# Kernel tuning notes

Measured on AMD Instinct MI355X. Metric: run time of the kernel, lower is better.

The kernel has to match this reference:

```python
import jax, jax.numpy as jnp
import numpy as np

B, T, D, H = 4, 2048, 1024, 16
HD = D // H  # 64


def setup_inputs() -> dict:
    key = jax.random.key(0)
    ks = jax.random.split(key, 6)
    s = 0.02
    return {
        "embed": jax.random.normal(ks[0], (B, T, D), dtype=jnp.float32),
        "mask": jnp.ones((1, 1, 1, T), dtype=jnp.int32),
        "Wq": jax.random.normal(ks[1], (D, D), dtype=jnp.float32) * s,
        "bq": jnp.zeros((D,), dtype=jnp.float32),
        "Wk": jax.random.normal(ks[2], (D, D), dtype=jnp.float32) * s,
        "bk": jnp.zeros((D,), dtype=jnp.float32),
        "Wv": jax.random.normal(ks[3], (D, D), dtype=jnp.float32) * s,
        "bv": jnp.zeros((D,), dtype=jnp.float32),
        "Wo": jax.random.normal(ks[4], (D, D), dtype=jnp.float32) * s,
        "bo": jnp.zeros((D,), dtype=jnp.float32),
    }


def _attn(embed, Wq, bq, Wk, bk, Wv, bv, Wo, bo, mask):
    b, t, _ = embed.shape
    q = (embed @ Wq + bq).reshape(b, t, H, HD).transpose(0, 2, 1, 3)  # [B,H,T,hd]
    k = (embed @ Wk + bk).reshape(b, t, H, HD).transpose(0, 2, 1, 3)
    v = (embed @ Wv + bv).reshape(b, t, H, HD).transpose(0, 2, 1, 3)
    scores = jnp.einsum("bhqd,bhkd->bhqk", q, k) * (1.0 / np.sqrt(HD))
    scores = jnp.where(mask == 0, jnp.float32(-jnp.inf), scores)
    weights = jax.nn.softmax(scores, axis=-1)  # dropout p=0 in eval
    ctx = jnp.einsum("bhqk,bhkd->bhqd", weights, v)
    merged = ctx.transpose(0, 2, 1, 3).reshape(b, t, D)
    return merged @ Wo + bo


def reference(embed, mask, Wq, bq, Wk, bk, Wv, bv, Wo, bo):
    return _attn(embed, Wq, bq, Wk, bk, Wv, bv, Wo, bo, mask)
```

## Files before the change

### kernel.cpp

```cpp
#include <hip/hip_runtime.h>


typedef __bf16 bf16_t;
typedef bf16_t bf16x8 __attribute__((ext_vector_type(8)));
typedef float  f32x4  __attribute__((ext_vector_type(4)));
typedef unsigned u32x4 __attribute__((ext_vector_type(4)));
typedef unsigned short u16x8 __attribute__((ext_vector_type(8)));
typedef unsigned short u16x4 __attribute__((ext_vector_type(4)));

#define DEV static __device__ __forceinline__

constexpr int Bc = 4, Tc = 2048, Dc = 1024, Hc = 16, HDc = 64;
constexpr int Mc = Bc * Tc;
constexpr int NQKV = 3 * Dc;

DEV unsigned short f2bf(float f) {
  union { float f; unsigned u; } v; v.f = f;
  return (unsigned short)((v.u + 0x7fffu + ((v.u >> 16) & 1u)) >> 16);
}

DEV void gload_lds16(const void* g, const void* ldsbase) {
  unsigned m0v = __builtin_amdgcn_readfirstlane((unsigned)(unsigned long long)ldsbase);
  asm volatile("s_mov_b32 m0, %0\n\t"
               "global_load_lds_dwordx4 %1, off"
               :: "s"(m0v), "v"(g) : "memory");
}

DEV f32x4 mfma16(bf16x8 a, bf16x8 b, f32x4 c) {
  return __builtin_amdgcn_mfma_f32_16x16x32_bf16(a, b, c, 0, 0, 0);
}

DEV void pl32swap(unsigned& a, unsigned& b) {
  asm("v_permlane32_swap_b32 %0, %1" : "+v"(a), "+v"(b));
}
DEV void pl16swap(unsigned& a, unsigned& b) {
  asm("v_permlane16_swap_b32 %0, %1" : "+v"(a), "+v"(b));
}

DEV int fragaddr(int row, int col) {
  return (row >> 4) * 1024 + ((col >> 5) << 9) + (((col >> 3) & 3) << 7)
       + ((row & 15) << 3) + (col & 7);
}

__global__ __launch_bounds__(256) void prep(const float* __restrict__ embed,
                                            const float* __restrict__ Wq,
                                            const float* __restrict__ Wk,
                                            const float* __restrict__ Wv,
                                            const float* __restrict__ Wo,
                                            const float* __restrict__ bq,
                                            const float* __restrict__ bk,
                                            const float* __restrict__ bv,
                                            unsigned short* __restrict__ embed_bf,
                                            unsigned short* __restrict__ WtAll,
                                            float* __restrict__ ball) {
  __shared__ unsigned short tile[64 * 80];
  const int bb = blockIdx.x;
  const int tid = threadIdx.x;

  if (bb < 8192) {
    int i = bb * 256 + tid;
    float4 v = ((const float4*)embed)[i];
    u16x4 o = { f2bf(v.x), f2bf(v.y), f2bf(v.z), f2bf(v.w) };
    *(u16x4*)(embed_bf + (size_t)i * 4) = o;
    return;
  }
  if (bb < 8192 + 1024) {
    int wb = bb - 8192;
    int bx = wb & 15, by = (wb >> 4) & 15, bz = wb >> 8;
    const float* W = bz == 0 ? Wq : bz == 1 ? Wk : bz == 2 ? Wv : Wo;
    unsigned short* dst = WtAll + (size_t)bz * 1024 * 1024;
    const int kb = by * 64, nb = bx * 64;
#pragma unroll
    for (int i = 0; i < 4; i++) {
      int ci = i * 256 + tid;
      int r = ci >> 4, c4 = ci & 15;
      float4 v = *(const float4*)(W + (size_t)(kb + r) * 1024 + nb + c4 * 4);
      u16x4 o = { f2bf(v.x), f2bf(v.y), f2bf(v.z), f2bf(v.w) };
      *(u16x4*)(tile + r * 80 + c4 * 4) = o;
    }
    __syncthreads();
#pragma unroll
    for (int i = 0; i < 2; i++) {
      int ci = i * 256 + tid;
      int n = ci >> 3, c8 = ci & 7;
      u16x8 o;
#pragma unroll
      for (int j = 0; j < 8; j++) o[j] = tile[(c8 * 8 + j) * 80 + n];
      *(u16x8*)(dst + (size_t)(nb + n) * 1024 + kb + c8 * 8) = o;
    }
    return;
  }
#pragma unroll
  for (int it = 0; it < 12; it++) {
    int i = it * 256 + tid;
    ball[i] = (i < 1024) ? bq[i] : (i < 2048) ? bk[i - 1024] : bv[i - 2048];
  }
}

__global__ __launch_bounds__(512, 2) void gemm_qkv8(
    const unsigned short* __restrict__ A,
    const unsigned short* __restrict__ Bt,
    const float* __restrict__ bias,
    unsigned short* __restrict__ Qf,
    unsigned short* __restrict__ Kf,
    unsigned short* __restrict__ Vf) {
  __shared__ unsigned short As_[4 * 8192];
  __shared__ unsigned short Bs_[4 * 8192];

  const int tid = threadIdx.x;
  const int lane = tid & 63, wid = tid >> 6;
  const int lr = lane & 15, lg = lane >> 4;
  const int wr = wid >> 2, wc = wid & 3;

  const int lin = blockIdx.y * 12 + blockIdx.x;
  const int swz = (lin & 7) * 48 + (lin >> 3);
  const int m0 = (swz / 12) * 256, n0 = (swz % 12) * 256;

  size_t gA[2], gB[2];
  int ldsoff[2];
#pragma unroll
  for (int i = 0; i < 2; i++) {
    int ci = i * 512 + tid;
    int row = ci >> 2;
    int cl = (ci & 3) ^ (row & 3);
    gA[i] = (size_t)(m0 + row) * 1024 + cl * 8;
    gB[i] = (size_t)(n0 + row) * 1024 + cl * 8;
    ldsoff[i] = ci * 8;
  }

  int offA[2][4], offB[4];
#pragma unroll
  for (int mq = 0; mq < 2; mq++)
#pragma unroll
    for (int m = 0; m < 4; m++) {
      int row = wr * 128 + mq * 64 + m * 16 + lr;
      offA[mq][m] = row * 32 + ((lg ^ (row & 3)) << 3);
    }
#pragma unroll
  for (int n = 0; n < 4; n++) {
    int row = wc * 64 + n * 16 + lr;
    offB[n] = row * 32 + ((lg ^ (row & 3)) << 3);
  }

  f32x4 acc[8][4] = {};

#define QSTAGE(kt) {                                                         \
    const int sbi_ = (kt) & 3;                                               \
    _Pragma("unroll")                                                        \
    for (int i_ = 0; i_ < 2; i_++) {                                         \
      gload_lds16(A  + gA[i_] + (size_t)(kt) * 32,                           \
                  As_ + sbi_ * 8192 + ldsoff[i_]);                           \
      gload_lds16(Bt + gB[i_] + (size_t)(kt) * 32,                           \
                  Bs_ + sbi_ * 8192 + ldsoff[i_]);                           \
    } }

#define QKTILE(kt, VM, DOST) {                                               \
    const int bi_ = (kt) & 3;                                                \
    const unsigned short* Ab = As_ + bi_ * 8192;                             \
    const unsigned short* Bb = Bs_ + bi_ * 8192;                             \
    asm volatile("s_waitcnt vmcnt(" VM ")" ::: "memory");                    \
    asm volatile("s_barrier" ::: "memory");                                  \
    bf16x8 a0 = *(const bf16x8*)(Ab + offA[0][0]);                           \
    bf16x8 a1 = *(const bf16x8*)(Ab + offA[0][1]);                           \
    bf16x8 a2 = *(const bf16x8*)(Ab + offA[0][2]);                           \
    bf16x8 a3 = *(const bf16x8*)(Ab + offA[0][3]);                           \
    bf16x8 b0 = *(const bf16x8*)(Bb + offB[0]);                              \
    bf16x8 b1 = *(const bf16x8*)(Bb + offB[1]);                              \
    bf16x8 b2 = *(const bf16x8*)(Bb + offB[2]);                              \
    bf16x8 b3 = *(const bf16x8*)(Bb + offB[3]);                              \
    if (DOST) QSTAGE((kt) + 3);                                              \
    __builtin_amdgcn_s_setprio(1);                                           \
    acc[0][0]=mfma16(a0,b0,acc[0][0]); acc[0][1]=mfma16(a0,b1,acc[0][1]);    \
    acc[0][2]=mfma16(a0,b2,acc[0][2]); acc[0][3]=mfma16(a0,b3,acc[0][3]);    \
    acc[1][0]=mfma16(a1,b0,acc[1][0]); acc[1][1]=mfma16(a1,b1,acc[1][1]);    \
    acc[1][2]=mfma16(a1,b2,acc[1][2]); acc[1][3]=mfma16(a1,b3,acc[1][3]);    \
    acc[2][0]=mfma16(a2,b0,acc[2][0]); acc[2][1]=mfma16(a2,b1,acc[2][1]);    \
    acc[2][2]=mfma16(a2,b2,acc[2][2]); acc[2][3]=mfma16(a2,b3,acc[2][3]);    \
    acc[3][0]=mfma16(a3,b0,acc[3][0]); acc[3][1]=mfma16(a3,b1,acc[3][1]);    \
    acc[3][2]=mfma16(a3,b2,acc[3][2]); acc[3][3]=mfma16(a3,b3,acc[3][3]);    \
    __builtin_amdgcn_s_setprio(0);                                           \
    a0 = *(const bf16x8*)(Ab + offA[1][0]);                                  \
    a1 = *(const bf16x8*)(Ab + offA[1][1]);                                  \
    a2 = *(const bf16x8*)(Ab + offA[1][2]);                                  \
    a3 = *(const bf16x8*)(Ab + offA[1][3]);                                  \
    __builtin_amdgcn_s_setprio(1);                                           \
    acc[4][0]=mfma16(a0,b0,acc[4][0]); acc[4][1]=mfma16(a0,b1,acc[4][1]);    \
    acc[4][2]=mfma16(a0,b2,acc[4][2]); acc[4][3]=mfma16(a0,b3,acc[4][3]);    \
    acc[5][0]=mfma16(a1,b0,acc[5][0]); acc[5][1]=mfma16(a1,b1,acc[5][1]);    \
    acc[5][2]=mfma16(a1,b2,acc[5][2]); acc[5][3]=mfma16(a1,b3,acc[5][3]);    \
    acc[6][0]=mfma16(a2,b0,acc[6][0]); acc[6][1]=mfma16(a2,b1,acc[6][1]);    \
    acc[6][2]=mfma16(a2,b2,acc[6][2]); acc[6][3]=mfma16(a2,b3,acc[6][3]);    \
    acc[7][0]=mfma16(a3,b0,acc[7][0]); acc[7][1]=mfma16(a3,b1,acc[7][1]);    \
    acc[7][2]=mfma16(a3,b2,acc[7][2]); acc[7][3]=mfma16(a3,b3,acc[7][3]);    \
    __builtin_amdgcn_s_setprio(0); }

  QSTAGE(0); QSTAGE(1); QSTAGE(2);

#pragma unroll 1
  for (int kt = 0; kt < 29; ++kt) {
    QKTILE(kt, "8", 1);
  }
  QKTILE(29, "8", 0);
  QKTILE(30, "4", 0);
  QKTILE(31, "0", 0);
#undef QSTAGE
#undef QKTILE

#pragma unroll
  for (int mq = 0; mq < 8; mq++)
#pragma unroll
    for (int n = 0; n < 4; n++)
#pragma unroll
      for (int r = 0; r < 4; r++) {
        int row = m0 + wr * 128 + (mq >> 2) * 64 + (mq & 3) * 16 + lg * 4 + r;
        int col = n0 + wc * 64 + n * 16 + lr;
        float v = acc[mq][n][r] + bias[col];
        int bb = row >> 11, tl = row & 2047;
        if (col < Dc) {
          v *= 0.18033688f;
          int h = col >> 6, d = col & 63;
          Qf[(size_t)(bb * 16 + h) * 131072 + fragaddr(tl, d)] = f2bf(v);
        } else if (col < 2 * Dc) {
          int c = col - Dc, h = c >> 6, d = c & 63;
          Kf[(size_t)(bb * 16 + h) * 131072 + fragaddr(tl, d)] = f2bf(v);
        } else {
          int c = col - 2 * Dc, h = c >> 6, d = c & 63;
          Vf[(size_t)(bb * 16 + h) * 131072 + (tl >> 6) * 4096 + fragaddr(d, tl & 63)] = f2bf(v);
        }
      }
}

__global__ __launch_bounds__(256) void gemm_bt(const unsigned short* __restrict__ A,
                                               const unsigned short* __restrict__ Bt,
                                               const float* __restrict__ bias,
                                               float* __restrict__ Cout,
                                               int N, int K) {
  __shared__ unsigned short As[128 * 64];
  __shared__ unsigned short Bs[128 * 64];
  const int tid = threadIdx.x;
  const int lane = tid & 63, wid = tid >> 6;
  const int lr = lane & 15, lg = lane >> 4;
  const int wrow = wid >> 1, wcol = wid & 1;
  const int m0 = blockIdx.y * 128, n0 = blockIdx.x * 128;

  f32x4 acc[4][4] = {};

  for (int k0 = 0; k0 < K; k0 += 64) {
#pragma unroll
    for (int i = 0; i < 4; i++) {
      int ci = i * 256 + tid;
      int row = ci >> 3, ph = ci & 7;
      int cl = ph ^ (row & 7);
      gload_lds16(A + (size_t)(m0 + row) * K + k0 + cl * 8, As + (size_t)(i * 256 + wid * 64) * 8);
      gload_lds16(Bt + (size_t)(n0 + row) * K + k0 + cl * 8, Bs + (size_t)(i * 256 + wid * 64) * 8);
    }
    asm volatile("s_waitcnt vmcnt(0)" ::: "memory");
    __syncthreads();
#pragma unroll
    for (int kk = 0; kk < 2; kk++) {
      bf16x8 av[4], bv[4];
#pragma unroll
      for (int m = 0; m < 4; m++) {
        int row = wrow * 64 + m * 16 + lr;
        int ph = (kk * 4 + lg) ^ (row & 7);
        av[m] = *(const bf16x8*)(As + row * 64 + ph * 8);
      }
#pragma unroll
      for (int n = 0; n < 4; n++) {
        int row = wcol * 64 + n * 16 + lr;
        int ph = (kk * 4 + lg) ^ (row & 7);
        bv[n] = *(const bf16x8*)(Bs + row * 64 + ph * 8);
      }
#pragma unroll
      for (int m = 0; m < 4; m++)
#pragma unroll
        for (int n = 0; n < 4; n++)
          acc[m][n] = mfma16(av[m], bv[n], acc[m][n]);
    }
    __syncthreads();
  }

#pragma unroll
  for (int m = 0; m < 4; m++)
#pragma unroll
    for (int n = 0; n < 4; n++)
#pragma unroll
      for (int r = 0; r < 4; r++) {
        int row = m0 + wrow * 64 + m * 16 + lg * 4 + r;
        int col = n0 + wcol * 64 + n * 16 + lr;
        Cout[(size_t)row * N + col] = acc[m][n][r] + bias[col];
      }
}

__global__ __launch_bounds__(256, 2) void flash7(const unsigned short* __restrict__ Qf,
                                                 const unsigned short* __restrict__ Kf,
                                                 const unsigned short* __restrict__ Vf,
                                                 const int* __restrict__ mask,
                                                 unsigned short* __restrict__ merged) {
  const int tid = threadIdx.x;
  const int lane = tid & 63, wid = tid >> 6;
  const int lr = lane & 15, lg = lane >> 4;

  const int lin = blockIdx.y * 8 + blockIdx.x;
  const int swz = (lin & 7) * 64 + (lin >> 3);
  const int qb = swz & 7, bh = swz >> 3;
  const int b = bh >> 4, h = bh & 15;
  const int wq = qb * 256 + wid * 64;

  const unsigned short* Qb = Qf + (size_t)bh * 131072;
  const unsigned short* Kb = Kf + (size_t)bh * 131072;
  const unsigned short* Vb = Vf + (size_t)bh * 131072;

  bf16x8 qf[4][2];
#pragma unroll
  for (int qn = 0; qn < 4; qn++)
#pragma unroll
    for (int kk = 0; kk < 2; kk++)
      qf[qn][kk] = *(const bf16x8*)(Qb + ((wq >> 4) + qn) * 1024 + kk * 512 + lane * 8);

  f32x4 o[4][4] = {};
  f32x4 lacc[4] = {};

  bf16x8 ones;
#pragma unroll
  for (int j = 0; j < 8; j++) ones[j] = (bf16_t)1.0f;

  bool allone = true;
#pragma unroll
  for (int j = 0; j < 8; j++) {
    int4 mv = ((const int4*)mask)[j * 64 + lane];
    allone = allone && (mv.x != 0) && (mv.y != 0) && (mv.z != 0) && (mv.w != 0);
  }
  const bool nomask = (__ballot(allone) == ~0ull);

#pragma unroll 2
  for (int tile = 0; tile < 32; tile++) {
    bf16x8 kf[4][2];
#pragma unroll
    for (int n = 0; n < 4; n++)
#pragma unroll
      for (int kk = 0; kk < 2; kk++)
        kf[n][kk] = *(const bf16x8*)(Kb + (tile * 4 + n) * 1024 + kk * 512 + lane * 8);
    bf16x8 vf[4][2];
#pragma unroll
    for (int dn = 0; dn < 4; dn++)
#pragma unroll
      for (int kk = 0; kk < 2; kk++)
        vf[dn][kk] = *(const bf16x8*)(Vb + tile * 4096 + dn * 1024 + kk * 512 + lane * 8);

    unsigned long long mb = ~0ull;
    if (!nomask) mb = __ballot(mask[tile * 64 + lane] != 0);

    unsigned pk[4][4][2];
#pragma unroll
    for (int kvn = 0; kvn < 4; kvn++) {
      f32x4 st[4] = {};
#pragma unroll
      for (int qn = 0; qn < 4; qn++) {
        st[qn] = mfma16(kf[kvn][0], qf[qn][0], st[qn]);
        st[qn] = mfma16(kf[kvn][1], qf[qn][1], st[qn]);
      }
      if (mb != ~0ull) {
#pragma unroll
        for (int r = 0; r < 4; r++)
          if (!((mb >> (kvn * 16 + lg * 4 + r)) & 1ull)) {
#pragma unroll
            for (int qn = 0; qn < 4; qn++) st[qn][r] = -1e30f;
          }
      }
#pragma unroll
      for (int qn = 0; qn < 4; qn++) {
        float e[4];
#pragma unroll
        for (int r = 0; r < 4; r++)
          asm("v_exp_f32 %0, %1" : "=v"(e[r]) : "v"(st[qn][r]));
        asm("v_cvt_pk_bf16_f32 %0, %1, %2" : "=v"(pk[qn][kvn][0]) : "v"(e[0]), "v"(e[1]));
        asm("v_cvt_pk_bf16_f32 %0, %1, %2" : "=v"(pk[qn][kvn][1]) : "v"(e[2]), "v"(e[3]));
      }
    }

    bf16x8 pa[4][2];
#pragma unroll
    for (int qn = 0; qn < 4; qn++)
#pragma unroll
      for (int m = 0; m < 2; m++) {
        unsigned a0 = pk[qn][2 * m][0], b0 = pk[qn][2 * m + 1][0];
        unsigned a1 = pk[qn][2 * m][1], b1 = pk[qn][2 * m + 1][1];
        pl32swap(a0, b0);
        pl32swap(a1, b1);
        pl16swap(a0, b0);
        pl16swap(a1, b1);
        u32x4 w = { a0, a1, b0, b1 };
        pa[qn][m] = __builtin_bit_cast(bf16x8, w);
      }

    __builtin_amdgcn_s_setprio(1);
#pragma unroll
    for (int qn = 0; qn < 4; qn++) {
#pragma unroll
      for (int dn = 0; dn < 4; dn++) {
        o[qn][dn] = mfma16(pa[qn][0], vf[dn][0], o[qn][dn]);
        o[qn][dn] = mfma16(pa[qn][1], vf[dn][1], o[qn][dn]);
      }
      lacc[qn] = mfma16(pa[qn][0], ones, lacc[qn]);
      lacc[qn] = mfma16(pa[qn][1], ones, lacc[qn]);
    }
    __builtin_amdgcn_s_setprio(0);
  }

#pragma unroll
  for (int qn = 0; qn < 4; qn++)
#pragma unroll
    for (int r = 0; r < 4; r++) {
      float inv = 1.0f / lacc[qn][r];
      int grow = b * Tc + wq + qn * 16 + lg * 4 + r;
#pragma unroll
      for (int dn = 0; dn < 4; dn++) {
        int gcol = h * HDc + dn * 16 + lr;
        merged[(size_t)grow * Dc + gcol] = f2bf(o[qn][dn][r] * inv);
      }
    }
}

extern "C" void kernel_launch(void* const* d_in, const int* in_sizes, int n_in,
                              void* d_out, int out_size, void* d_ws, size_t ws_size,
                              hipStream_t stream) {
  const float* embed = (const float*)d_in[0];
  const int*   mask  = (const int*)d_in[1];
  const float* Wq = (const float*)d_in[2];
  const float* bq = (const float*)d_in[3];
  const float* Wk = (const float*)d_in[4];
  const float* bk = (const float*)d_in[5];
  const float* Wv = (const float*)d_in[6];
  const float* bv = (const float*)d_in[7];
  const float* Wo = (const float*)d_in[8];
  const float* bo = (const float*)d_in[9];
  float* out = (float*)d_out;

  char* ws = (char*)d_ws;
  unsigned short* embed_bf = (unsigned short*)ws; ws += (size_t)Mc * Dc * 2;
  unsigned short* WtAll    = (unsigned short*)ws; ws += (size_t)4 * Dc * Dc * 2;
  float*          ball     = (float*)ws;          ws += 16384;
  unsigned short* Qf       = (unsigned short*)ws; ws += (size_t)Mc * Dc * 2;
  unsigned short* Kf       = (unsigned short*)ws; ws += (size_t)Mc * Dc * 2;
  unsigned short* Vf       = (unsigned short*)ws; ws += (size_t)Mc * Dc * 2;
  unsigned short* merged   = (unsigned short*)ws; ws += (size_t)Mc * Dc * 2;

  prep<<<8192 + 1024 + 1, 256, 0, stream>>>(embed, Wq, Wk, Wv, Wo, bq, bk, bv,
                                            embed_bf, WtAll, ball);
  gemm_qkv8<<<dim3(12, 32), 512, 0, stream>>>(embed_bf, WtAll, ball, Qf, Kf, Vf);
  flash7<<<dim3(8, 64), 256, 0, stream>>>(Qf, Kf, Vf, mask, merged);
  gemm_bt<<<dim3(8, 64), 256, 0, stream>>>(merged, WtAll + (size_t)3 * Dc * Dc, bo, out, Dc, Dc);
}
```

Baseline: 192.6 us.

## Restructure QKV GEMM main loop with K=64 double-buffered tiles and staged sub-phases

The QKV projection GEMM now uses 64-wide K tiles in a double-buffered LDS ring instead of a 4-deep ring of 32-wide tiles. The global-to-LDS stage is split into four quarter-tile loads that are interleaved between four MFMA sub-phases of each K-tile. Each sub-phase is fenced with lgkmcnt waits and barriers, in the style of HipKittens-like 8-wave ping-pong scheduling. The goal is to halve the loop trip count and overlap loads with MFMA more evenly, at the cost of more barriers per iteration and a 128 KB LDS footprint, which may limit occupancy to one block per CU.

Result: slower. 198.3 us (+3.0%).

```diff
diff --git a/kernel.cpp b/kernel.cpp
--- a/kernel.cpp
+++ b/kernel.cpp
@@ -97,15 +97,15 @@
   }
 }
 
-__global__ __launch_bounds__(512, 2) void gemm_qkv8(
+__global__ __launch_bounds__(512, 2) void gemm_qkv9(
     const unsigned short* __restrict__ A,
     const unsigned short* __restrict__ Bt,
     const float* __restrict__ bias,
     unsigned short* __restrict__ Qf,
     unsigned short* __restrict__ Kf,
     unsigned short* __restrict__ Vf) {
-  __shared__ unsigned short As_[4 * 8192];
-  __shared__ unsigned short Bs_[4 * 8192];
+  __shared__ unsigned short LA[32768];
+  __shared__ unsigned short LB[32768];
 
   const int tid = threadIdx.x;
   const int lane = tid & 63, wid = tid >> 6;
@@ -116,105 +116,118 @@
   const int swz = (lin & 7) * 48 + (lin >> 3);
   const int m0 = (swz / 12) * 256, n0 = (swz % 12) * 256;
 
-  size_t gA[2], gB[2];
-  int ldsoff[2];
+  int srow[2], scl[2], sdst[2];
 #pragma unroll
   for (int i = 0; i < 2; i++) {
     int ci = i * 512 + tid;
-    int row = ci >> 2;
-    int cl = (ci & 3) ^ (row & 3);
-    gA[i] = (size_t)(m0 + row) * 1024 + cl * 8;
-    gB[i] = (size_t)(n0 + row) * 1024 + cl * 8;
-    ldsoff[i] = ci * 8;
-  }
-
-  int offA[2][4], offB[4];
-#pragma unroll
-  for (int mq = 0; mq < 2; mq++)
-#pragma unroll
-    for (int m = 0; m < 4; m++) {
-      int row = wr * 128 + mq * 64 + m * 16 + lr;
-      offA[mq][m] = row * 32 + ((lg ^ (row & 3)) << 3);
-    }
-#pragma unroll
-  for (int n = 0; n < 4; n++) {
-    int row = wc * 64 + n * 16 + lr;
-    offB[n] = row * 32 + ((lg ^ (row & 3)) << 3);
-  }
-
-  f32x4 acc[8][4] = {};
-
-#define QSTAGE(kt) {                                                         \
-    const int sbi_ = (kt) & 3;                                               \
+    srow[i] = ci >> 3;
+    scl[i] = (ci & 7) ^ (srow[i] & 7);
+    sdst[i] = ci * 8;
+  }
+
+#define STG(s_) {                                                            \
+    const int ts_ = (s_) >> 2, j_ = (s_) & 3, d_ = ts_ & 1;                  \
     _Pragma("unroll")                                                        \
     for (int i_ = 0; i_ < 2; i_++) {                                         \
-      gload_lds16(A  + gA[i_] + (size_t)(kt) * 32,                           \
-                  As_ + sbi_ * 8192 + ldsoff[i_]);                           \
-      gload_lds16(Bt + gB[i_] + (size_t)(kt) * 32,                           \
-                  Bs_ + sbi_ * 8192 + ldsoff[i_]);                           \
+      if (j_ < 2)                                                            \
+        gload_lds16(A + (size_t)(m0 + j_ * 128 + srow[i_]) * 1024            \
+                      + ts_ * 64 + scl[i_] * 8,                              \
+                    LA + (d_ * 2 + j_) * 8192 + sdst[i_]);                   \
+      else                                                                   \
+        gload_lds16(Bt + (size_t)(n0 + (j_ - 2) * 128 + srow[i_]) * 1024     \
+                       + ts_ * 64 + scl[i_] * 8,                             \
+                    LB + (d_ * 2 + (j_ - 2)) * 8192 + sdst[i_]);             \
     } }
 
-#define QKTILE(kt, VM, DOST) {                                               \
-    const int bi_ = (kt) & 3;                                                \
-    const unsigned short* Ab = As_ + bi_ * 8192;                             \
-    const unsigned short* Bb = Bs_ + bi_ * 8192;                             \
-    asm volatile("s_waitcnt vmcnt(" VM ")" ::: "memory");                    \
-    asm volatile("s_barrier" ::: "memory");                                  \
-    bf16x8 a0 = *(const bf16x8*)(Ab + offA[0][0]);                           \
-    bf16x8 a1 = *(const bf16x8*)(Ab + offA[0][1]);                           \
-    bf16x8 a2 = *(const bf16x8*)(Ab + offA[0][2]);                           \
-    bf16x8 a3 = *(const bf16x8*)(Ab + offA[0][3]);                           \
-    bf16x8 b0 = *(const bf16x8*)(Bb + offB[0]);                              \
-    bf16x8 b1 = *(const bf16x8*)(Bb + offB[1]);                              \
-    bf16x8 b2 = *(const bf16x8*)(Bb + offB[2]);                              \
-    bf16x8 b3 = *(const bf16x8*)(Bb + offB[3]);                              \
-    if (DOST) QSTAGE((kt) + 3);                                              \
+  const int aoff = lr * 64;
+  const int co0 = (lg ^ (lr & 7)) << 3;
+  const int co1 = ((4 + lg) ^ (lr & 7)) << 3;
+  const int bhalf = (wc & 1) * 4096;
+
+  f32x4 acc[8][4] = {};
+  bf16x8 aR[4][2], bR[4][2];
+
+#define RD_A(Ad_, mbase_) {                                                  \
+    _Pragma("unroll")                                                        \
+    for (int m_ = 0; m_ < 4; m_++) {                                         \
+      aR[m_][0] = *(const bf16x8*)((Ad_) + ((mbase_) + m_) * 1024 + aoff + co0); \
+      aR[m_][1] = *(const bf16x8*)((Ad_) + ((mbase_) + m_) * 1024 + aoff + co1); \
+    } }
+#define RD_B(Bd_, nlo_) {                                                    \
+    _Pragma("unroll")                                                        \
+    for (int n_ = 0; n_ < 2; n_++) {                                         \
+      bR[(nlo_) + n_][0] = *(const bf16x8*)((Bd_) + bhalf + ((nlo_) + n_) * 1024 + aoff + co0); \
+      bR[(nlo_) + n_][1] = *(const bf16x8*)((Bd_) + bhalf + ((nlo_) + n_) * 1024 + aoff + co1); \
+    } }
+#define MFMA16(mb_, nl_) {                                                   \
     __builtin_amdgcn_s_setprio(1);                                           \
-    acc[0][0]=mfma16(a0,b0,acc[0][0]); acc[0][1]=mfma16(a0,b1,acc[0][1]);    \
-    acc[0][2]=mfma16(a0,b2,acc[0][2]); acc[0][3]=mfma16(a0,b3,acc[0][3]);    \
-    acc[1][0]=mfma16(a1,b0,acc[1][0]); acc[1][1]=mfma16(a1,b1,acc[1][1]);    \
-    acc[1][2]=mfma16(a1,b2,acc[1][2]); acc[1][3]=mfma16(a1,b3,acc[1][3]);    \
-    acc[2][0]=mfma16(a2,b0,acc[2][0]); acc[2][1]=mfma16(a2,b1,acc[2][1]);    \
-    acc[2][2]=mfma16(a2,b2,acc[2][2]); acc[2][3]=mfma16(a2,b3,acc[2][3]);    \
-    acc[3][0]=mfma16(a3,b0,acc[3][0]); acc[3][1]=mfma16(a3,b1,acc[3][1]);    \
-    acc[3][2]=mfma16(a3,b2,acc[3][2]); acc[3][3]=mfma16(a3,b3,acc[3][3]);    \
-    __builtin_amdgcn_s_setprio(0);                                           \
-    a0 = *(const bf16x8*)(Ab + offA[1][0]);                                  \
-    a1 = *(const bf16x8*)(Ab + offA[1][1]);                                  \
-    a2 = *(const bf16x8*)(Ab + offA[1][2]);                                  \
-    a3 = *(const bf16x8*)(Ab + offA[1][3]);                                  \
-    __builtin_amdgcn_s_setprio(1);                                           \
-    acc[4][0]=mfma16(a0,b0,acc[4][0]); acc[4][1]=mfma16(a0,b1,acc[4][1]);    \
-    acc[4][2]=mfma16(a0,b2,acc[4][2]); acc[4][3]=mfma16(a0,b3,acc[4][3]);    \
-    acc[5][0]=mfma16(a1,b0,acc[5][0]); acc[5][1]=mfma16(a1,b1,acc[5][1]);    \
-    acc[5][2]=mfma16(a1,b2,acc[5][2]); acc[5][3]=mfma16(a1,b3,acc[5][3]);    \
-    acc[6][0]=mfma16(a2,b0,acc[6][0]); acc[6][1]=mfma16(a2,b1,acc[6][1]);    \
-    acc[6][2]=mfma16(a2,b2,acc[6][2]); acc[6][3]=mfma16(a2,b3,acc[6][3]);    \
-    acc[7][0]=mfma16(a3,b0,acc[7][0]); acc[7][1]=mfma16(a3,b1,acc[7][1]);    \
-    acc[7][2]=mfma16(a3,b2,acc[7][2]); acc[7][3]=mfma16(a3,b3,acc[7][3]);    \
+    _Pragma("unroll")                                                        \
+    for (int m_ = 0; m_ < 4; m_++)                                           \
+      _Pragma("unroll")                                                      \
+      for (int n_ = 0; n_ < 2; n_++) {                                       \
+        acc[(mb_) + m_][(nl_) + n_] =                                        \
+            mfma16(aR[m_][0], bR[(nl_) + n_][0], acc[(mb_) + m_][(nl_) + n_]); \
+        acc[(mb_) + m_][(nl_) + n_] =                                        \
+            mfma16(aR[m_][1], bR[(nl_) + n_][1], acc[(mb_) + m_][(nl_) + n_]); \
+      }                                                                      \
     __builtin_amdgcn_s_setprio(0); }
 
-  QSTAGE(0); QSTAGE(1); QSTAGE(2);
+#define LGKM0 { asm volatile("s_waitcnt lgkmcnt(0)" ::: "memory");           \
+                __builtin_amdgcn_sched_barrier(0); }
+#define BAR   { asm volatile("s_barrier" ::: "memory"); }
+
+#define KTILE(kt_, DO01, DO2, DO3, DOVM, VMq3) {                             \
+    const unsigned short* Ad = LA + wr * 8192 + ((kt_) & 1) * 16384;         \
+    const unsigned short* Bd = LB + (wc >> 1) * 8192 + ((kt_) & 1) * 16384;  \
+                                                                     \
+    RD_A(Ad, 0); RD_B(Bd, 0);                                                \
+    LGKM0; BAR;                                                              \
+    if (DO01) STG(4 * (kt_) + 6);                                            \
+    MFMA16(0, 0); BAR;                                                       \
+                                                                     \
+    RD_B(Bd, 2);                                                             \
+    LGKM0; BAR;                                                              \
+    if (DO01) STG(4 * (kt_) + 7);                                            \
+    MFMA16(0, 2); BAR;                                                       \
+                                                                     \
+    RD_A(Ad, 4);                                                             \
+    LGKM0; BAR;                                                              \
+    if (DO2) STG(4 * (kt_) + 8);                                             \
+    MFMA16(4, 0); BAR;                                                       \
+                                                                     \
+    if (DO3) STG(4 * (kt_) + 9);                                             \
+    MFMA16(4, 2);                                                            \
+    if (DOVM) { asm volatile("s_waitcnt vmcnt(" VMq3 ")" ::: "memory"); }    \
+    BAR; }
+
+  STG(0); STG(1); STG(2); STG(3); STG(4); STG(5);
+  asm volatile("s_waitcnt vmcnt(4)" ::: "memory");
+  BAR;
 
 #pragma unroll 1
-  for (int kt = 0; kt < 29; ++kt) {
-    QKTILE(kt, "8", 1);
-  }
-  QKTILE(29, "8", 0);
-  QKTILE(30, "4", 0);
-  QKTILE(31, "0", 0);
-#undef QSTAGE
-#undef QKTILE
-
-#pragma unroll
-  for (int mq = 0; mq < 8; mq++)
+  for (int kt = 0; kt < 14; ++kt) {
+    KTILE(kt, 1, 1, 1, 1, "4");
+  }
+  KTILE(14, 1, 0, 0, 1, "0");
+  KTILE(15, 0, 0, 0, 0, "0");
+
+#undef KTILE
+#undef BAR
+#undef LGKM0
+#undef MFMA16
+#undef RD_B
+#undef RD_A
+#undef STG
+
+#pragma unroll
+  for (int m = 0; m < 8; m++)
 #pragma unroll
     for (int n = 0; n < 4; n++)
 #pragma unroll
       for (int r = 0; r < 4; r++) {
-        int row = m0 + wr * 128 + (mq >> 2) * 64 + (mq & 3) * 16 + lg * 4 + r;
+        int row = m0 + wr * 128 + m * 16 + lg * 4 + r;
         int col = n0 + wc * 64 + n * 16 + lr;
-        float v = acc[mq][n][r] + bias[col];
+        float v = acc[m][n][r] + bias[col];
         int bb = row >> 11, tl = row & 2047;
         if (col < Dc) {
           v *= 0.18033688f;
@@ -448,7 +461,7 @@
 
   prep<<<8192 + 1024 + 1, 256, 0, stream>>>(embed, Wq, Wk, Wv, Wo, bq, bk, bv,
                                             embed_bf, WtAll, ball);
-  gemm_qkv8<<<dim3(12, 32), 512, 0, stream>>>(embed_bf, WtAll, ball, Qf, Kf, Vf);
+  gemm_qkv9<<<dim3(12, 32), 512, 0, stream>>>(embed_bf, WtAll, ball, Qf, Kf, Vf);
   flash7<<<dim3(8, 64), 256, 0, stream>>>(Qf, Kf, Vf, mask, merged);
   gemm_bt<<<dim3(8, 64), 256, 0, stream>>>(merged, WtAll + (size_t)3 * Dc * Dc, bo, out, Dc, Dc);
 }
```
